# Optimization experiments

Hardware: AMD Instinct MI355X
Metric: run time of the kernel (lower is better)

The kernel has to match this reference:

```python
import jax, jax.numpy as jnp
import numpy as np

EMBED_DIM = 1024
NUM_HEADS = 16
HEAD_DIM = EMBED_DIM // NUM_HEADS


def setup_inputs() -> dict:
    key = jax.random.key(0)
    kx, kq, kk, kv, ko = jax.random.split(key, 5)
    B, S = 4, 2048
    std = 1.0 / np.sqrt(EMBED_DIM)
    x = jax.random.normal(kx, (B, S, EMBED_DIM), dtype=jnp.float32)
    # nn.Linear weights stored as [out, in]; applied as x @ W.T
    Wq = jax.random.normal(kq, (EMBED_DIM, EMBED_DIM), dtype=jnp.float32) * std
    Wk = jax.random.normal(kk, (EMBED_DIM, EMBED_DIM), dtype=jnp.float32) * std
    Wv = jax.random.normal(kv, (EMBED_DIM, EMBED_DIM), dtype=jnp.float32) * std
    Wo = jax.random.normal(ko, (EMBED_DIM, EMBED_DIM), dtype=jnp.float32) * std
    return {"x": x, "Wq": Wq, "Wk": Wk, "Wv": Wv, "Wo": Wo}


def reference(x, Wq, Wk, Wv, Wo):
    B, S, E = x.shape
    H, D = NUM_HEADS, HEAD_DIM
    scale = jnp.sqrt(jnp.float32(D))

    def proj(W):
        # x @ W.T -> (B, S, E) -> (B, H, S, D)
        return (x @ W.T).reshape(B, S, H, D).transpose(0, 2, 1, 3)

    q, k, v = proj(Wq), proj(Wk), proj(Wv)
    scores = jnp.einsum("bhsd,bhtd->bhst", q, k) / scale  # (B,H,S,S)
    causal = jnp.tril(jnp.ones((S, S), dtype=bool))
    scores = jnp.where(causal, scores, -jnp.inf)
    attn = jax.nn.softmax(scores, axis=-1)  # dropout in eval mode = identity
    out = jnp.einsum("bhst,bhtd->bhsd", attn, v)  # (B,H,S,D)
    out = out.transpose(0, 2, 1, 3).reshape(B, S, E)
    return out @ Wo.T
```

## Files before the change

### kernel.cpp

```cpp
#include <hip/hip_runtime.h>
#include <stdint.h>

#define NHEADS 16
#define EDIM   1024
#define SEQ    2048
#define BATCH  4

typedef float  floatx4 __attribute__((ext_vector_type(4)));
typedef __bf16 bf16x8  __attribute__((ext_vector_type(8)));
typedef unsigned short u16;

__device__ __forceinline__ u16 f2bf(float f) {
  union { float f; unsigned int u; } v; v.f = f;
  return (u16)((v.u + 0x7fffu + ((v.u >> 16) & 1u)) >> 16);
}

__device__ __forceinline__ unsigned int pkbf(float lo, float hi) {
  union { float f; unsigned int u; } a, c;
  a.f = lo; c.f = hi;
  return __builtin_amdgcn_perm(c.u + 0x8000u, a.u + 0x8000u, 0x07060302u);
}

__device__ __forceinline__ void gl2lds16(const u16* g, u16* l) {
  __builtin_amdgcn_global_load_lds(
      (const __attribute__((address_space(1))) unsigned int*)g,
      (__attribute__((address_space(3))) unsigned int*)l, 16, 0, 0);
}

__global__ void cvt_all(const float* __restrict__ x,  const float* __restrict__ wq,
                        const float* __restrict__ wk, const float* __restrict__ wv,
                        const float* __restrict__ wo, u16* __restrict__ xb,
                        u16* __restrict__ wqkv, u16* __restrict__ wob, float qscale) {
  const float* src; u16* dst; int n4; float sc = 1.f;
  switch (blockIdx.y) {
    case 0: src = x;  dst = xb;             n4 = 2097152; break;
    case 1: src = wq; dst = wqkv;           n4 = 262144; sc = qscale; break;
    case 2: src = wk; dst = wqkv + 1048576; n4 = 262144; break;
    case 3: src = wv; dst = wqkv + 2097152; n4 = 262144; break;
    default: src = wo; dst = wob;           n4 = 262144; break;
  }
  const int stride = gridDim.x * blockDim.x;
  for (int i = blockIdx.x * blockDim.x + threadIdx.x; i < n4; i += stride) {
    float4 f = ((const float4*)src)[i];
    uint2 o;
    o.x = pkbf(f.x * sc, f.y * sc);
    o.y = pkbf(f.z * sc, f.w * sc);
    ((uint2*)dst)[i] = o;
  }
}

__global__ __launch_bounds__(512, 4)
void gemm_qkv(const u16* __restrict__ A, const u16* __restrict__ B,
              u16* __restrict__ Cq, u16* __restrict__ Ck, u16* __restrict__ Cv) {
  constexpr int SLOT = (128 + 256) * 32;
  constexpr int BOFF = 128 * 32;
  __shared__ __align__(16) u16 ring[3][SLOT];
  const int tid  = threadIdx.x;
  const int w    = tid >> 6, lane = tid & 63;
  const int quad = lane >> 4, l15 = lane & 15;
  const int wrow = (w >> 2) * 64, bcol = (w & 3) * 64;

  const int f  = (int)blockIdx.x;
  const int g  = f >> 3;
  const int bx = (f & 7) * 4 + (g & 3);
  const int by = g >> 2;
  const int rowA0 = by * 128, rowB0 = bx * 256;
  const int matid = rowA0 >> 10;

  const int cp = lane & 3;
  const int ra = w * 16 + (lane >> 2);
  const u16* srcA  = A + (size_t)(rowA0 + ra) * 1024 + (cp ^ ((ra >> 1) & 3)) * 8;
  const int rb0 = w * 32 + (lane >> 2);
  const u16* srcB0 = B + (size_t)(rowB0 + rb0) * 1024 + (cp ^ ((rb0 >> 1) & 3)) * 8;
  const u16* srcB1 = srcB0 + 16 * 1024;

#define STG(sl, tt)                                                          \
  {                                                                          \
    const int _ko = (tt) * 32;                                               \
    gl2lds16(srcA + _ko, &ring[sl][0] + w * 512);                            \
    gl2lds16(srcB0 + _ko, &ring[sl][BOFF] + w * 1024);                       \
    gl2lds16(srcB1 + _ko, &ring[sl][BOFF] + w * 1024 + 512);                 \
  }

  const floatx4 vzero = {0.f, 0.f, 0.f, 0.f};
  floatx4 acc[4][4];
#pragma unroll
  for (int mi = 0; mi < 4; ++mi)
#pragma unroll
    for (int ni = 0; ni < 4; ++ni) acc[mi][ni] = vzero;

  const int swz8 = (quad ^ ((l15 >> 1) & 3)) * 8;
  constexpr int NT = 32;
  STG(0, 0);
  STG(1, 1);
  int cs = 0, ss = 2;

#define KLOOP(SWAPPED)                                                       \
  for (int t = 0; t < NT; ++t) {                                             \
    if (t < NT - 1) asm volatile("s_waitcnt vmcnt(3)" ::: "memory");         \
    else            asm volatile("s_waitcnt vmcnt(0)" ::: "memory");         \
    __builtin_amdgcn_s_barrier();                                            \
    if (t + 2 < NT) { STG(ss, t + 2); ss = (ss == 2) ? 0 : ss + 1; }         \
    const u16* As = &ring[cs][0];                                            \
    const u16* Bs = &ring[cs][BOFF];                                         \
    cs = (cs == 2) ? 0 : cs + 1;                                             \
    bf16x8 af[4], bfr[4];                                                    \
    _Pragma("unroll")                                                        \
    for (int j = 0; j < 4; ++j)                                              \
      af[j] = *(const bf16x8*)(As + (wrow + j * 16 + l15) * 32 + swz8);      \
    _Pragma("unroll")                                                        \
    for (int nj = 0; nj < 4; ++nj)                                           \
      bfr[nj] = *(const bf16x8*)(Bs + (bcol + nj * 16 + l15) * 32 + swz8);   \
    __builtin_amdgcn_s_setprio(1);                                           \
    _Pragma("unroll")                                                        \
    for (int mi = 0; mi < 4; ++mi)                                           \
      _Pragma("unroll")                                                      \
      for (int ni = 0; ni < 4; ++ni) {                                       \
        if (SWAPPED)                                                         \
          acc[mi][ni] = __builtin_amdgcn_mfma_f32_16x16x32_bf16(             \
              bfr[ni], af[mi], acc[mi][ni], 0, 0, 0);                        \
        else                                                                 \
          acc[mi][ni] = __builtin_amdgcn_mfma_f32_16x16x32_bf16(             \
              af[mi], bfr[ni], acc[mi][ni], 0, 0, 0);                        \
      }                                                                      \
    __builtin_amdgcn_s_setprio(0);                                           \
  }

  if (matid < 2) {
    KLOOP(0)
    u16* dst = (matid == 0) ? Cq : Ck;
#pragma unroll
    for (int mi = 0; mi < 4; ++mi)
#pragma unroll
      for (int ni = 0; ni < 4; ++ni) {
        const int e0 = rowA0 + wrow + mi * 16 + quad * 4;
        const int s  = rowB0 + bcol + ni * 16 + l15;
        const int e_loc = e0 & 1023;
        uint2 pk;
        pk.x = pkbf(acc[mi][ni][0], acc[mi][ni][1]);
        pk.y = pkbf(acc[mi][ni][2], acc[mi][ni][3]);
        *(uint2*)(dst + (size_t)s * 1024 + e_loc) = pk;
      }
  } else {
    KLOOP(1)
#pragma unroll
    for (int mi = 0; mi < 4; ++mi)
#pragma unroll
      for (int ni = 0; ni < 4; ++ni) {
        const int e_loc = (rowA0 & 1023) + wrow + mi * 16 + l15;
        const int s_full = rowB0 + bcol + ni * 16 + quad * 4;
        const int pos = (s_full & ~31) | (quad << 3) | ((ni & 1) << 2);
        const int bb = pos >> 11, pos_loc = pos & 2047;
        uint2 pk;
        pk.x = pkbf(acc[mi][ni][0], acc[mi][ni][1]);
        pk.y = pkbf(acc[mi][ni][2], acc[mi][ni][3]);
        *(uint2*)(Cv + (size_t)(bb * 1024 + e_loc) * SEQ + pos_loc) = pk;
      }
  }
#undef KLOOP
#undef STG
}

__global__ __launch_bounds__(512, 4)
void gemm_out(const u16* __restrict__ A, const u16* __restrict__ B,
              float* __restrict__ C) {
  constexpr int SLOT = 256 * 32;
  constexpr int BOFF = 128 * 32;
  __shared__ __align__(16) u16 ring[3][SLOT];
  const int tid  = threadIdx.x;
  const int w    = tid >> 6, lane = tid & 63;
  const int quad = lane >> 4, l15 = lane & 15;
  const int wrow = (w >> 2) * 64, bcol = (w & 3) * 32;

  const int f  = (int)blockIdx.x;
  const int g  = f >> 3;
  const int bx = (f & 7) * 8 + (g & 7);
  const int by = g >> 3;
  const int rowA0 = by * 128, rowB0 = bx * 128;

  const int cp = lane & 3;
  const int ra = w * 16 + (lane >> 2);
  const u16* srcA  = A + (size_t)(rowA0 + ra) * 1024 + (cp ^ ((ra >> 1) & 3)) * 8;
  const u16* srcB0 = B + (size_t)(rowB0 + ra) * 1024 + (cp ^ ((ra >> 1) & 3)) * 8;

#define STG(sl, tt)                                                          \
  {                                                                          \
    const int _ko = (tt) * 32;                                               \
    gl2lds16(srcA + _ko, &ring[sl][0] + w * 512);                            \
    gl2lds16(srcB0 + _ko, &ring[sl][BOFF] + w * 512);                        \
  }

  const floatx4 vzero = {0.f, 0.f, 0.f, 0.f};
  floatx4 acc[4][2];
#pragma unroll
  for (int mi = 0; mi < 4; ++mi)
#pragma unroll
    for (int ni = 0; ni < 2; ++ni) acc[mi][ni] = vzero;

  const int swz8 = (quad ^ ((l15 >> 1) & 3)) * 8;
  constexpr int NT = 32;
  STG(0, 0);
  STG(1, 1);
  int cs = 0, ss = 2;

  for (int t = 0; t < NT; ++t) {
    if (t < NT - 1) asm volatile("s_waitcnt vmcnt(2)" ::: "memory");
    else            asm volatile("s_waitcnt vmcnt(0)" ::: "memory");
    __builtin_amdgcn_s_barrier();
    if (t + 2 < NT) { STG(ss, t + 2); ss = (ss == 2) ? 0 : ss + 1; }

    const u16* As = &ring[cs][0];
    const u16* Bs = &ring[cs][BOFF];
    cs = (cs == 2) ? 0 : cs + 1;
    bf16x8 af[4], bfr[2];
#pragma unroll
    for (int j = 0; j < 4; ++j)
      af[j] = *(const bf16x8*)(As + (wrow + j * 16 + l15) * 32 + swz8);
#pragma unroll
    for (int nj = 0; nj < 2; ++nj)
      bfr[nj] = *(const bf16x8*)(Bs + (bcol + nj * 16 + l15) * 32 + swz8);
    __builtin_amdgcn_s_setprio(1);
#pragma unroll
    for (int mi = 0; mi < 4; ++mi)
#pragma unroll
      for (int ni = 0; ni < 2; ++ni)
        acc[mi][ni] = __builtin_amdgcn_mfma_f32_16x16x32_bf16(af[mi], bfr[ni], acc[mi][ni], 0, 0, 0);
    __builtin_amdgcn_s_setprio(0);
  }
#undef STG

#pragma unroll
  for (int mi = 0; mi < 4; ++mi)
#pragma unroll
    for (int ni = 0; ni < 2; ++ni) {
      const int e0 = rowA0 + wrow + mi * 16 + quad * 4;
      const int s  = rowB0 + bcol + ni * 16 + l15;
      *(floatx4*)(C + (size_t)s * 1024 + e0) = acc[mi][ni];
    }
}

__global__ __launch_bounds__(512, 4)
void attn_fwd(const u16* __restrict__ Q, const u16* __restrict__ K,
              const u16* __restrict__ Vp, u16* __restrict__ Ctx) {
  __shared__ u16 SMEM[4 * 8192];
  const int tid  = threadIdx.x;
  const int w    = tid >> 6, lane = tid & 63;
  const int quad = lane >> 4, l15 = lane & 15;
  const int qg = w >> 1, tg = w & 1;
  const int bh = blockIdx.x, b = bh >> 4, h = bh & 15;
  const int qt = 15 - (int)blockIdx.y;
  const int kmax = qt;
  const int q0 = qt * 128 + qg * 32;

  bf16x8 bq[2][2];
#pragma unroll
  for (int ni = 0; ni < 2; ++ni)
#pragma unroll
    for (int ks = 0; ks < 2; ++ks) {
      const int qs = q0 + ni * 16 + l15;
      bq[ni][ks] = *(const bf16x8*)(Q + (size_t)(b * SEQ + qs) * EDIM + h * 64 + ks * 32 + quad * 8);
    }

  const floatx4 vzero = {0.f, 0.f, 0.f, 0.f};
  floatx4 o_acc[4][2];
  float l_acc[2] = {0.f, 0.f};
#pragma unroll
  for (int di = 0; di < 4; ++di)
#pragma unroll
    for (int ni = 0; ni < 2; ++ni) o_acc[di][ni] = vzero;

  const int krow = lane >> 3, kch = lane & 7;
  const int vrow = lane >> 4, vch = lane & 15;

#define STAGE_KV(buf, ktn)                                                          \
  {                                                                                 \
    _Pragma("unroll")                                                               \
    for (int ii = 0; ii < 2; ++ii) {                                                \
      const int r0 = w * 16 + ii * 8;                                               \
      const int row = r0 + krow;                                                    \
      gl2lds16(K + (size_t)(b * SEQ + (ktn) * 128 + row) * EDIM + h * 64 +          \
                   ((kch ^ (row & 7)) * 8),                                         \
               SMEM + (buf) * 8192 + r0 * 64);                                      \
      const int d0 = w * 8 + ii * 4;                                                \
      const int dd = d0 + vrow;                                                     \
      gl2lds16(Vp + (size_t)(bh * 64 + dd) * SEQ + (ktn) * 128 +                    \
                   ((vch ^ (dd & 15)) * 8),                                         \
               SMEM + 16384 + (buf) * 8192 + d0 * 128);                             \
    }                                                                               \
  }

  STAGE_KV(0, 0);

  for (int kt = 0; kt <= kmax; ++kt) {
    const int cur = kt & 1;
    __syncthreads();
    if (kt < kmax) STAGE_KV(cur ^ 1, kt + 1);
    const u16* Ksc = SMEM + cur * 8192;
    const u16* Vsc = SMEM + 16384 + cur * 8192;

    unsigned int pk[2][2][4];
#pragma unroll
    for (int mi = 0; mi < 4; ++mi) {
      floatx4 s[2] = {vzero, vzero};
#pragma unroll
      for (int ks = 0; ks < 2; ++ks) {
        bf16x8 ak = *(const bf16x8*)(Ksc + (tg * 64 + mi * 16 + l15) * 64 +
                                     (((ks * 4 + quad) ^ (l15 & 7)) * 8));
#pragma unroll
        for (int ni = 0; ni < 2; ++ni)
          s[ni] = __builtin_amdgcn_mfma_f32_16x16x32_bf16(ak, bq[ni][ks], s[ni], 0, 0, 0);
      }
      if (kt == kmax) {
#pragma unroll
        for (int ni = 0; ni < 2; ++ni)
#pragma unroll
          for (int r = 0; r < 4; ++r) {
            const int t_loc = tg * 64 + mi * 16 + quad * 4 + r;
            const int q_loc = qg * 32 + ni * 16 + l15;
            if (t_loc > q_loc) s[ni][r] = -1e30f;
          }
      }
#pragma unroll
      for (int ni = 0; ni < 2; ++ni) {
        float p0 = __builtin_amdgcn_exp2f(s[ni][0]);
        float p1 = __builtin_amdgcn_exp2f(s[ni][1]);
        float p2 = __builtin_amdgcn_exp2f(s[ni][2]);
        float p3 = __builtin_amdgcn_exp2f(s[ni][3]);
        l_acc[ni] += (p0 + p1) + (p2 + p3);
        pk[ni][mi >> 1][(mi & 1) * 2 + 0] = pkbf(p0, p1);
        pk[ni][mi >> 1][(mi & 1) * 2 + 1] = pkbf(p2, p3);
      }
    }

#pragma unroll
    for (int ks = 0; ks < 2; ++ks) {
      bf16x8 va[4];
#pragma unroll
      for (int di = 0; di < 4; ++di)
        va[di] = *(const bf16x8*)(Vsc + (di * 16 + l15) * 128 +
                                  (((tg * 8 + ks * 4 + quad) ^ l15) * 8));
#pragma unroll
      for (int ni = 0; ni < 2; ++ni) {
        union { unsigned int u[4]; bf16x8 v; } pb;
        pb.u[0] = pk[ni][ks][0]; pb.u[1] = pk[ni][ks][1];
        pb.u[2] = pk[ni][ks][2]; pb.u[3] = pk[ni][ks][3];
#pragma unroll
        for (int di = 0; di < 4; ++di)
          o_acc[di][ni] = __builtin_amdgcn_mfma_f32_16x16x32_bf16(va[di], pb.v, o_acc[di][ni], 0, 0, 0);
      }
    }
  }

  float lt[2];
#pragma unroll
  for (int ni = 0; ni < 2; ++ni) {
    float v = l_acc[ni];
    v += __shfl_xor(v, 16, 64);
    v += __shfl_xor(v, 32, 64);
    lt[ni] = v;
  }
  __syncthreads();
  float* red  = (float*)SMEM;
  float* lred = red + 8448;
  if (tg == 1) {
#pragma unroll
    for (int ni = 0; ni < 2; ++ni) {
#pragma unroll
      for (int di = 0; di < 4; ++di)
#pragma unroll
        for (int r = 0; r < 4; ++r)
          red[qg * 2112 + (di * 16 + quad * 4 + r) * 33 + ni * 16 + l15] = o_acc[di][ni][r];
      if (quad == 0) lred[qg * 32 + ni * 16 + l15] = lt[ni];
    }
  }
  __syncthreads();
  if (tg == 0) {
#pragma unroll
    for (int ni = 0; ni < 2; ++ni) {
      const float rl = 1.f / (lt[ni] + lred[qg * 32 + ni * 16 + l15]);
      const int qs = q0 + ni * 16 + l15;
#pragma unroll
      for (int di = 0; di < 4; ++di) {
        float v0 = (o_acc[di][ni][0] + red[qg * 2112 + (di * 16 + quad * 4 + 0) * 33 + ni * 16 + l15]) * rl;
        float v1 = (o_acc[di][ni][1] + red[qg * 2112 + (di * 16 + quad * 4 + 1) * 33 + ni * 16 + l15]) * rl;
        float v2 = (o_acc[di][ni][2] + red[qg * 2112 + (di * 16 + quad * 4 + 2) * 33 + ni * 16 + l15]) * rl;
        float v3 = (o_acc[di][ni][3] + red[qg * 2112 + (di * 16 + quad * 4 + 3) * 33 + ni * 16 + l15]) * rl;
        uint2 ov;
        ov.x = pkbf(v0, v1);
        ov.y = pkbf(v2, v3);
        *(uint2*)(Ctx + (size_t)(b * SEQ + qs) * EDIM + h * 64 + di * 16 + quad * 4) = ov;
      }
    }
  }
#undef STAGE_KV
}

extern "C" void kernel_launch(void* const* d_in, const int* in_sizes, int n_in,
                              void* d_out, int out_size, void* d_ws, size_t ws_size,
                              hipStream_t stream) {
  const float* x  = (const float*)d_in[0];
  const float* Wq = (const float*)d_in[1];
  const float* Wk = (const float*)d_in[2];
  const float* Wv = (const float*)d_in[3];
  const float* Wo = (const float*)d_in[4];
  float* out = (float*)d_out;
  u16* ws = (u16*)d_ws;

  const size_t ME = (size_t)BATCH * SEQ * EDIM;
  u16* Xb   = ws;
  u16* Wqkv = Xb + ME;
  u16* Wob  = Wqkv + 3u * 1024 * 1024;
  u16* Qb   = Wob + 1024u * 1024;
  u16* Kb   = Qb + ME;
  u16* Vpb  = Kb + ME;
  u16* Ctx  = Vpb + ME;

  const float qscale = 0.125f * 1.44269504f;

  cvt_all<<<dim3(512, 5), 256, 0, stream>>>(x, Wq, Wk, Wv, Wo, Xb, Wqkv, Wob, qscale);
  gemm_qkv<<<dim3(768), 512, 0, stream>>>(Wqkv, Xb, Qb, Kb, Vpb);
  attn_fwd<<<dim3(64, 16), 512, 0, stream>>>(Qb, Kb, Vpb, Ctx);
  gemm_out<<<dim3(512), 512, 0, stream>>>(Wob, Ctx, out);
}
```

Measured before the change: 218.3 us.

## Use 4-wave blocks with larger per-wave tiles in QKV and output GEMMs

Both projection GEMMs move from 8-wave (512-thread) blocks to 4-wave (256-thread) blocks, and each wave now owns a larger output tile. In gemm_qkv each wave computes 128x64 (32 accumulators). In gemm_out the block tile changes from 128x128 to 64x256, with each wave computing 64x64. The aim is more MFMA work per LDS fragment read and fewer waves contending for the barrier. The cost is higher register pressure (acc[8][4] is 128 VGPRs), fewer waves to hide latency, and more global-to-LDS loads issued per wave, with the vmcnt waits adjusted to match.

```diff
diff --git a/kernel.cpp b/kernel.cpp
--- a/kernel.cpp
+++ b/kernel.cpp
@@ -49,7 +49,7 @@
   }
 }
 
-__global__ __launch_bounds__(512, 4)
+__global__ __launch_bounds__(256, 2)
 void gemm_qkv(const u16* __restrict__ A, const u16* __restrict__ B,
               u16* __restrict__ Cq, u16* __restrict__ Ck, u16* __restrict__ Cv) {
   constexpr int SLOT = (128 + 256) * 32;
@@ -58,7 +58,7 @@
   const int tid  = threadIdx.x;
   const int w    = tid >> 6, lane = tid & 63;
   const int quad = lane >> 4, l15 = lane & 15;
-  const int wrow = (w >> 2) * 64, bcol = (w & 3) * 64;
+  const int bcol = w * 64;
 
   const int f  = (int)blockIdx.x;
   const int g  = f >> 3;
@@ -68,24 +68,26 @@
   const int matid = rowA0 >> 10;
 
   const int cp = lane & 3;
-  const int ra = w * 16 + (lane >> 2);
+  const int ra = w * 32 + (lane >> 2);
   const u16* srcA  = A + (size_t)(rowA0 + ra) * 1024 + (cp ^ ((ra >> 1) & 3)) * 8;
-  const int rb0 = w * 32 + (lane >> 2);
-  const u16* srcB0 = B + (size_t)(rowB0 + rb0) * 1024 + (cp ^ ((rb0 >> 1) & 3)) * 8;
-  const u16* srcB1 = srcB0 + 16 * 1024;
+  const int rb = w * 64 + (lane >> 2);
+  const u16* srcB  = B + (size_t)(rowB0 + rb) * 1024 + (cp ^ ((rb >> 1) & 3)) * 8;
 
 #define STG(sl, tt)                                                          \
   {                                                                          \
     const int _ko = (tt) * 32;                                               \
-    gl2lds16(srcA + _ko, &ring[sl][0] + w * 512);                            \
-    gl2lds16(srcB0 + _ko, &ring[sl][BOFF] + w * 1024);                       \
-    gl2lds16(srcB1 + _ko, &ring[sl][BOFF] + w * 1024 + 512);                 \
+    gl2lds16(srcA + _ko,             &ring[sl][0] + w * 1024);               \
+    gl2lds16(srcA + 16 * 1024 + _ko, &ring[sl][0] + w * 1024 + 512);         \
+    _Pragma("unroll")                                                        \
+    for (int jj = 0; jj < 4; ++jj)                                           \
+      gl2lds16(srcB + jj * 16 * 1024 + _ko,                                  \
+               &ring[sl][BOFF] + w * 2048 + jj * 512);                       \
   }
 
   const floatx4 vzero = {0.f, 0.f, 0.f, 0.f};
-  floatx4 acc[4][4];
-#pragma unroll
-  for (int mi = 0; mi < 4; ++mi)
+  floatx4 acc[8][4];
+#pragma unroll
+  for (int mi = 0; mi < 8; ++mi)
 #pragma unroll
     for (int ni = 0; ni < 4; ++ni) acc[mi][ni] = vzero;
 
@@ -97,23 +99,23 @@
 
 #define KLOOP(SWAPPED)                                                       \
   for (int t = 0; t < NT; ++t) {                                             \
-    if (t < NT - 1) asm volatile("s_waitcnt vmcnt(3)" ::: "memory");         \
+    if (t < NT - 1) asm volatile("s_waitcnt vmcnt(6)" ::: "memory");         \
     else            asm volatile("s_waitcnt vmcnt(0)" ::: "memory");         \
     __builtin_amdgcn_s_barrier();                                            \
     if (t + 2 < NT) { STG(ss, t + 2); ss = (ss == 2) ? 0 : ss + 1; }         \
     const u16* As = &ring[cs][0];                                            \
     const u16* Bs = &ring[cs][BOFF];                                         \
     cs = (cs == 2) ? 0 : cs + 1;                                             \
-    bf16x8 af[4], bfr[4];                                                    \
+    bf16x8 af[8], bfr[4];                                                    \
     _Pragma("unroll")                                                        \
-    for (int j = 0; j < 4; ++j)                                              \
-      af[j] = *(const bf16x8*)(As + (wrow + j * 16 + l15) * 32 + swz8);      \
+    for (int j = 0; j < 8; ++j)                                              \
+      af[j] = *(const bf16x8*)(As + (j * 16 + l15) * 32 + swz8);             \
     _Pragma("unroll")                                                        \
     for (int nj = 0; nj < 4; ++nj)                                           \
       bfr[nj] = *(const bf16x8*)(Bs + (bcol + nj * 16 + l15) * 32 + swz8);   \
     __builtin_amdgcn_s_setprio(1);                                           \
     _Pragma("unroll")                                                        \
-    for (int mi = 0; mi < 4; ++mi)                                           \
+    for (int mi = 0; mi < 8; ++mi)                                           \
       _Pragma("unroll")                                                      \
       for (int ni = 0; ni < 4; ++ni) {                                       \
         if (SWAPPED)                                                         \
@@ -130,10 +132,10 @@
     KLOOP(0)
     u16* dst = (matid == 0) ? Cq : Ck;
 #pragma unroll
-    for (int mi = 0; mi < 4; ++mi)
+    for (int mi = 0; mi < 8; ++mi)
 #pragma unroll
       for (int ni = 0; ni < 4; ++ni) {
-        const int e0 = rowA0 + wrow + mi * 16 + quad * 4;
+        const int e0 = rowA0 + mi * 16 + quad * 4;
         const int s  = rowB0 + bcol + ni * 16 + l15;
         const int e_loc = e0 & 1023;
         uint2 pk;
@@ -144,10 +146,10 @@
   } else {
     KLOOP(1)
 #pragma unroll
-    for (int mi = 0; mi < 4; ++mi)
+    for (int mi = 0; mi < 8; ++mi)
 #pragma unroll
       for (int ni = 0; ni < 4; ++ni) {
-        const int e_loc = (rowA0 & 1023) + wrow + mi * 16 + l15;
+        const int e_loc = (rowA0 & 1023) + mi * 16 + l15;
         const int s_full = rowB0 + bcol + ni * 16 + quad * 4;
         const int pos = (s_full & ~31) | (quad << 3) | ((ni & 1) << 2);
         const int bb = pos >> 11, pos_loc = pos & 2047;
@@ -161,41 +163,45 @@
 #undef STG
 }
 
-__global__ __launch_bounds__(512, 4)
+__global__ __launch_bounds__(256, 2)
 void gemm_out(const u16* __restrict__ A, const u16* __restrict__ B,
               float* __restrict__ C) {
-  constexpr int SLOT = 256 * 32;
-  constexpr int BOFF = 128 * 32;
+  constexpr int SLOT = (64 + 256) * 32;
+  constexpr int BOFF = 64 * 32;
   __shared__ __align__(16) u16 ring[3][SLOT];
   const int tid  = threadIdx.x;
   const int w    = tid >> 6, lane = tid & 63;
   const int quad = lane >> 4, l15 = lane & 15;
-  const int wrow = (w >> 2) * 64, bcol = (w & 3) * 32;
+  const int bcol = w * 64;
 
   const int f  = (int)blockIdx.x;
   const int g  = f >> 3;
-  const int bx = (f & 7) * 8 + (g & 7);
-  const int by = g >> 3;
-  const int rowA0 = by * 128, rowB0 = bx * 128;
+  const int bx = (f & 7) * 4 + (g & 3);
+  const int by = g >> 2;
+  const int rowA0 = by * 64, rowB0 = bx * 256;
 
   const int cp = lane & 3;
   const int ra = w * 16 + (lane >> 2);
-  const u16* srcA  = A + (size_t)(rowA0 + ra) * 1024 + (cp ^ ((ra >> 1) & 3)) * 8;
-  const u16* srcB0 = B + (size_t)(rowB0 + ra) * 1024 + (cp ^ ((ra >> 1) & 3)) * 8;
+  const u16* srcA = A + (size_t)(rowA0 + ra) * 1024 + (cp ^ ((ra >> 1) & 3)) * 8;
+  const int rb = w * 64 + (lane >> 2);
+  const u16* srcB = B + (size_t)(rowB0 + rb) * 1024 + (cp ^ ((rb >> 1) & 3)) * 8;
 
 #define STG(sl, tt)                                                          \
   {                                                                          \
     const int _ko = (tt) * 32;                                               \
     gl2lds16(srcA + _ko, &ring[sl][0] + w * 512);                            \
-    gl2lds16(srcB0 + _ko, &ring[sl][BOFF] + w * 512);                        \
+    _Pragma("unroll")                                                        \
+    for (int jj = 0; jj < 4; ++jj)                                           \
+      gl2lds16(srcB + jj * 16 * 1024 + _ko,                                  \
+               &ring[sl][BOFF] + w * 2048 + jj * 512);                       \
   }
 
   const floatx4 vzero = {0.f, 0.f, 0.f, 0.f};
-  floatx4 acc[4][2];
+  floatx4 acc[4][4];
 #pragma unroll
   for (int mi = 0; mi < 4; ++mi)
 #pragma unroll
-    for (int ni = 0; ni < 2; ++ni) acc[mi][ni] = vzero;
+    for (int ni = 0; ni < 4; ++ni) acc[mi][ni] = vzero;
 
   const int swz8 = (quad ^ ((l15 >> 1) & 3)) * 8;
   constexpr int NT = 32;
@@ -204,7 +210,7 @@
   int cs = 0, ss = 2;
 
   for (int t = 0; t < NT; ++t) {
-    if (t < NT - 1) asm volatile("s_waitcnt vmcnt(2)" ::: "memory");
+    if (t < NT - 1) asm volatile("s_waitcnt vmcnt(5)" ::: "memory");
     else            asm volatile("s_waitcnt vmcnt(0)" ::: "memory");
     __builtin_amdgcn_s_barrier();
     if (t + 2 < NT) { STG(ss, t + 2); ss = (ss == 2) ? 0 : ss + 1; }
@@ -212,18 +218,18 @@
     const u16* As = &ring[cs][0];
     const u16* Bs = &ring[cs][BOFF];
     cs = (cs == 2) ? 0 : cs + 1;
-    bf16x8 af[4], bfr[2];
+    bf16x8 af[4], bfr[4];
 #pragma unroll
     for (int j = 0; j < 4; ++j)
-      af[j] = *(const bf16x8*)(As + (wrow + j * 16 + l15) * 32 + swz8);
-#pragma unroll
-    for (int nj = 0; nj < 2; ++nj)
+      af[j] = *(const bf16x8*)(As + (j * 16 + l15) * 32 + swz8);
+#pragma unroll
+    for (int nj = 0; nj < 4; ++nj)
       bfr[nj] = *(const bf16x8*)(Bs + (bcol + nj * 16 + l15) * 32 + swz8);
     __builtin_amdgcn_s_setprio(1);
 #pragma unroll
     for (int mi = 0; mi < 4; ++mi)
 #pragma unroll
-      for (int ni = 0; ni < 2; ++ni)
+      for (int ni = 0; ni < 4; ++ni)
         acc[mi][ni] = __builtin_amdgcn_mfma_f32_16x16x32_bf16(af[mi], bfr[ni], acc[mi][ni], 0, 0, 0);
     __builtin_amdgcn_s_setprio(0);
   }
@@ -232,8 +238,8 @@
 #pragma unroll
   for (int mi = 0; mi < 4; ++mi)
 #pragma unroll
-    for (int ni = 0; ni < 2; ++ni) {
-      const int e0 = rowA0 + wrow + mi * 16 + quad * 4;
+    for (int ni = 0; ni < 4; ++ni) {
+      const int e0 = rowA0 + mi * 16 + quad * 4;
       const int s  = rowB0 + bcol + ni * 16 + l15;
       *(floatx4*)(C + (size_t)s * 1024 + e0) = acc[mi][ni];
     }
@@ -418,7 +424,7 @@
   const float qscale = 0.125f * 1.44269504f;
 
   cvt_all<<<dim3(512, 5), 256, 0, stream>>>(x, Wq, Wk, Wv, Wo, Xb, Wqkv, Wob, qscale);
-  gemm_qkv<<<dim3(768), 512, 0, stream>>>(Wqkv, Xb, Qb, Kb, Vpb);
+  gemm_qkv<<<dim3(768), 256, 0, stream>>>(Wqkv, Xb, Qb, Kb, Vpb);
   attn_fwd<<<dim3(64, 16), 512, 0, stream>>>(Qb, Kb, Vpb, Ctx);
-  gemm_out<<<dim3(512), 512, 0, stream>>>(Wob, Ctx, out);
-}
+  gemm_out<<<dim3(512), 256, 0, stream>>>(Wob, Ctx, out);
+}
```

Result: slower. 237.8 us (+8.9%).
